# Kernel tuning notes

Hardware: AMD Instinct MI355X
Metric: run time of the kernel (lower is better)

## Reference

```python
import jax, jax.numpy as jnp
import numpy as np

N = 100000      # num nodes
E = 1600000     # num edges
F_IN = 128
F_OUT = 128
BN_EPS = 1e-5


def setup_inputs() -> dict:
    key = jax.random.key(0)
    ks = jax.random.split(key, 8)
    x = jax.random.normal(ks[0], (N, F_IN), dtype=jnp.float32)
    edge_index = jax.random.randint(ks[1], (2, E), 0, N, dtype=jnp.int64)
    # GIN learnable epsilon (init 0.0)
    eps = jnp.zeros((), dtype=jnp.float32)
    # MLP: Linear(F_IN->F_OUT) -> BatchNorm1d -> ReLU -> Linear(F_OUT->F_OUT)
    lim1 = 1.0 / np.sqrt(F_IN)
    W1 = jax.random.uniform(ks[2], (F_OUT, F_IN), minval=-lim1, maxval=lim1, dtype=jnp.float32)
    b1 = jax.random.uniform(ks[3], (F_OUT,), minval=-lim1, maxval=lim1, dtype=jnp.float32)
    gamma = jnp.ones((F_OUT,), dtype=jnp.float32)
    beta = jnp.zeros((F_OUT,), dtype=jnp.float32)
    lim2 = 1.0 / np.sqrt(F_OUT)
    W2 = jax.random.uniform(ks[4], (F_OUT, F_OUT), minval=-lim2, maxval=lim2, dtype=jnp.float32)
    b2 = jax.random.uniform(ks[5], (F_OUT,), minval=-lim2, maxval=lim2, dtype=jnp.float32)
    return {"x": x, "edge_index": edge_index, "eps": eps,
            "W1": W1, "b1": b1, "gamma": gamma, "beta": beta,
            "W2": W2, "b2": b2}


def reference(x, edge_index, eps, W1, b1, gamma, beta, W2, b2):
    row, col = edge_index[0], edge_index[1]
    # gather neighbor features and scatter-add into destination nodes
    agg = jax.ops.segment_sum(x[col], row, num_segments=x.shape[0])  # [N, F_IN]
    h = (1.0 + eps) * x + agg
    # Linear 1
    h = h @ W1.T + b1  # [N, F_OUT]
    # BatchNorm1d (training mode: batch stats over nodes, biased variance)
    mu = jnp.mean(h, axis=0)
    var = jnp.mean(jnp.square(h - mu), axis=0)
    h = (h - mu) * jax.lax.rsqrt(var + BN_EPS) * gamma + beta
    h = jax.nn.relu(h)
    # Linear 2
    return h @ W2.T + b2
```

## Files before the change

### kernel.cpp

```cpp
#include <hip/hip_runtime.h>


#define F 128
#define NPB 64
#define CLCAP 3072

typedef __attribute__((ext_vector_type(8))) short short8;
typedef __attribute__((ext_vector_type(4))) float float4v;

__device__ inline float b2f(unsigned short u) {
    union { unsigned int i; float f; } v; v.i = ((unsigned int)u) << 16; return v.f;
}
__device__ inline unsigned short f2b(float f) {
    union { float f; unsigned int i; } v; v.f = f;
    unsigned int r = v.i + 0x7FFFu + ((v.i >> 16) & 1u);
    return (unsigned short)(r >> 16);
}

__global__ __launch_bounds__(256) void conv_kernel(const float* __restrict__ x,
                                                   unsigned short* __restrict__ xh, int total,
                                                   const float* __restrict__ W1,
                                                   const float* __restrict__ W2,
                                                   unsigned short* __restrict__ w1h,
                                                   unsigned short* __restrict__ w2h,
                                                   int* __restrict__ bucketCnt, int nbuk,
                                                   float* __restrict__ stats) {
    int t = blockIdx.x * 256 + threadIdx.x;
    int i = t * 8;
    if (i < total) {
        float4 v0 = *(const float4*)(x + i);
        float4 v1 = *(const float4*)(x + i + 4);
        short8 o;
        o[0] = (short)f2b(v0.x); o[1] = (short)f2b(v0.y); o[2] = (short)f2b(v0.z); o[3] = (short)f2b(v0.w);
        o[4] = (short)f2b(v1.x); o[5] = (short)f2b(v1.y); o[6] = (short)f2b(v1.z); o[7] = (short)f2b(v1.w);
        *(short8*)(xh + i) = o;
    }
    if (t < F * F) {
        w1h[t] = f2b(W1[t]);
        w2h[t] = f2b(W2[t]);
    }
    if (blockIdx.x == 0) {
        for (int k = threadIdx.x; k < nbuk; k += 256) bucketCnt[k] = 0;
    } else if (blockIdx.x == 1) {
        if (threadIdx.x < 256) stats[threadIdx.x] = 0.f;
    }
}

__global__ __launch_bounds__(256) void bucket_hist_kernel(const int* __restrict__ rows,
                                                          int* __restrict__ bucketCnt,
                                                          int E, int nbuk) {
    extern __shared__ int bh[];
    int tid = threadIdx.x;
    for (int i = tid; i < nbuk; i += 256) bh[i] = 0;
    __syncthreads();
    int stride = gridDim.x * 256;
    for (int i = blockIdx.x * 256 + tid; i < E; i += stride)
        atomicAdd(&bh[rows[i] >> 6], 1);
    __syncthreads();
    for (int b = tid; b < nbuk; b += 256) {
        int c = bh[b];
        if (c) atomicAdd(&bucketCnt[b], c);
    }
}

__global__ void scan_buckets_kernel(const int* __restrict__ bucketCnt, int* __restrict__ bOffs,
                                    int* __restrict__ gcursor, int nbuk) {
    const int SEG = 7;
    __shared__ int tmp[256];
    int t = threadIdx.x;
    int base = t * SEG;
    int v[SEG], s = 0;
#pragma unroll
    for (int j = 0; j < SEG; j++) {
        int idx = base + j;
        v[j] = (idx < nbuk) ? bucketCnt[idx] : 0;
        s += v[j];
    }
    tmp[t] = s;
    __syncthreads();
    for (int off = 1; off < 256; off <<= 1) {
        int u = (t >= off) ? tmp[t - off] : 0;
        __syncthreads();
        tmp[t] += u;
        __syncthreads();
    }
    int run = tmp[t] - s;
#pragma unroll
    for (int j = 0; j < SEG; j++) {
        int idx = base + j;
        if (idx < nbuk) { bOffs[idx] = run; gcursor[idx] = run; }
        run += v[j];
    }
    if (t == 255) bOffs[nbuk] = tmp[255];
}

__global__ __launch_bounds__(1024) void binned_scatter_kernel(const int* __restrict__ rows,
                                                              const int* __restrict__ cols,
                                                              int* __restrict__ gcursor,
                                                              int* __restrict__ recbuf,
                                                              int E, int nbuk) {
    extern __shared__ int sm[];
    int* bh = sm;
    int* gb = sm + nbuk;
    int tid = threadIdx.x;
    int chunk = (E + gridDim.x - 1) / gridDim.x;
    int e0 = blockIdx.x * chunk;
    int e1 = min(E, e0 + chunk);
    for (int i = tid; i < nbuk; i += 1024) bh[i] = 0;
    __syncthreads();
    for (int i = e0 + tid; i < e1; i += 1024)
        atomicAdd(&bh[rows[i] >> 6], 1);
    __syncthreads();
    for (int b = tid; b < nbuk; b += 1024) {
        int c = bh[b];
        gb[b] = c ? atomicAdd(&gcursor[b], c) : 0;
        bh[b] = 0;
    }
    __syncthreads();
    for (int i = e0 + tid; i < e1; i += 1024) {
        int r = rows[i], c = cols[i];
        int k = r >> 6;
        int rk = atomicAdd(&bh[k], 1);
        recbuf[gb[k] + rk] = (c << 6) | (r & 63);
    }
}

__global__ __launch_bounds__(256) void sort_agg_kernel(const int* __restrict__ recbuf,
                                                       const int* __restrict__ bOffs,
                                                       const unsigned short* __restrict__ xh,
                                                       const float* __restrict__ epsPtr,
                                                       unsigned short* __restrict__ h0h,
                                                       int* __restrict__ clist,
                                                       int n, int nbuk) {
    __shared__ int hist[NPB];
    __shared__ int cur[NPB];
    __shared__ int offs_s[NPB + 1];
    __shared__ int cl[CLCAP];
    int b = blockIdx.x, tid = threadIdx.x;
    int base = bOffs[b];
    int cnt = bOffs[b + 1] - base;
    if (tid < NPB) hist[tid] = 0;
    __syncthreads();
    for (int i = tid; i < cnt; i += 256) atomicAdd(&hist[recbuf[base + i] & 63], 1);
    __syncthreads();
    if (tid < 64) {
        int h = hist[tid], v = h;
#pragma unroll
        for (int off = 1; off < 64; off <<= 1) {
            int u = __shfl_up(v, off, 64);
            if (tid >= off) v += u;
        }
        cur[tid] = v - h;
        offs_s[tid] = v - h;
        if (tid == 63) offs_s[64] = v;
    }
    __syncthreads();
    bool inlds = (cnt <= CLCAP);
    if (inlds) {
        for (int i = tid; i < cnt; i += 256) {
            int r = recbuf[base + i];
            int p = atomicAdd(&cur[r & 63], 1);
            cl[p] = r >> 6;
        }
    } else {
        for (int i = tid; i < cnt; i += 256) {
            int r = recbuf[base + i];
            int p = atomicAdd(&cur[r & 63], 1);
            clist[base + p] = r >> 6;
        }
    }
    __syncthreads();

    int wv = tid >> 6, lane = tid & 63;
    int qt = lane >> 4;
    int c16 = lane & 15;
    const short8* xh8 = (const short8*)xh;
    float sc = 1.0f + epsPtr[0];
    const int* glist = clist + base;
    for (int nd = wv; nd < NPB; nd += 4) {
        int node = b * NPB + nd;
        if (node >= n) break;
        int s = offs_s[nd], e = offs_s[nd + 1];
        float acc[8];
#pragma unroll
        for (int j = 0; j < 8; j++) acc[j] = 0.f;
        int i = s;
        for (; i + 16 <= e; i += 16) {
            int c[4];
#pragma unroll
            for (int u = 0; u < 4; u++) {
                int idx = i + 4 * u + qt;
                c[u] = inlds ? cl[idx] : glist[idx];
            }
            short8 v[4];
#pragma unroll
            for (int u = 0; u < 4; u++) v[u] = xh8[(size_t)c[u] * 16 + c16];
#pragma unroll
            for (int u = 0; u < 4; u++)
#pragma unroll
                for (int j = 0; j < 8; j++) acc[j] += b2f((unsigned short)v[u][j]);
        }
        if (i < e) {
            int c[4];
#pragma unroll
            for (int u = 0; u < 4; u++) {
                int idx = i + 4 * u + qt;
                c[u] = (idx < e) ? (inlds ? cl[idx] : glist[idx]) : -1;
            }
            short8 v[4];
#pragma unroll
            for (int u = 0; u < 4; u++)
                v[u] = xh8[(size_t)(c[u] < 0 ? 0 : c[u]) * 16 + c16];
#pragma unroll
            for (int u = 0; u < 4; u++) {
                if (c[u] >= 0) {
#pragma unroll
                    for (int j = 0; j < 8; j++) acc[j] += b2f((unsigned short)v[u][j]);
                }
            }
        }
#pragma unroll
        for (int j = 0; j < 8; j++) {
            acc[j] += __shfl_xor(acc[j], 16, 64);
            acc[j] += __shfl_xor(acc[j], 32, 64);
        }
        if (qt == 0) {
            short8 xv = xh8[(size_t)node * 16 + c16];
            short8 o;
#pragma unroll
            for (int j = 0; j < 8; j++) {
                float r = fmaf(sc, b2f((unsigned short)xv[j]), acc[j]);
                o[j] = (short)f2b(r);
            }
            ((short8*)h0h)[(size_t)node * 16 + c16] = o;
        }
    }
}

#define WLD 136
__global__ __launch_bounds__(256, 2) void gemm1_mfma_kernel(const unsigned short* __restrict__ h0h,
                                                            const unsigned short* __restrict__ w1h,
                                                            const float* __restrict__ b1,
                                                            unsigned short* __restrict__ h1h,
                                                            float* __restrict__ stats, int n) {
    __shared__ unsigned short wl[128 * WLD];
    __shared__ float red[4 * 256];
    int tid = threadIdx.x;
    for (int i = tid; i < 128 * 16; i += 256) {
        int r = i >> 4, ch = i & 15;
        *(short8*)(wl + r * WLD + ch * 8) = *(const short8*)(w1h + r * 128 + ch * 8);
    }
    __syncthreads();

    int wv = tid >> 6, lane = tid & 63;
    int q = lane >> 4, c15 = lane & 15;
    int rowbase = blockIdx.x * 64 + wv * 16;
    int arow = rowbase + c15; if (arow >= n) arow = n - 1;
    const unsigned short* aptr = h0h + (size_t)arow * 128 + q * 8;

    float4v acc[8];
#pragma unroll
    for (int nt = 0; nt < 8; nt++) {
        float bb = b1[nt * 16 + c15];
        acc[nt] = (float4v){bb, bb, bb, bb};
    }
#pragma unroll
    for (int ks = 0; ks < 4; ks++) {
        short8 a = *(const short8*)(aptr + ks * 32);
        const unsigned short* wp = wl + q * 8 + ks * 32;
#pragma unroll
        for (int nt = 0; nt < 8; nt++) {
            short8 b = *(const short8*)(wp + (nt * 16 + c15) * WLD);
            acc[nt] = __builtin_amdgcn_mfma_f32_16x16x32_bf16(a, b, acc[nt], 0, 0, 0);
        }
    }

    float sum[8], sq[8];
#pragma unroll
    for (int nt = 0; nt < 8; nt++) {
        sum[nt] = 0.f; sq[nt] = 0.f;
#pragma unroll
        for (int r = 0; r < 4; r++) {
            int row = rowbase + q * 4 + r;
            if (row < n) {
                float v = acc[nt][r];
                h1h[(size_t)row * 128 + nt * 16 + c15] = f2b(v);
                sum[nt] += v; sq[nt] += v * v;
            }
        }
        sum[nt] += __shfl_xor(sum[nt], 16, 64);
        sum[nt] += __shfl_xor(sum[nt], 32, 64);
        sq[nt]  += __shfl_xor(sq[nt], 16, 64);
        sq[nt]  += __shfl_xor(sq[nt], 32, 64);
    }
    if (lane < 16) {
#pragma unroll
        for (int nt = 0; nt < 8; nt++) {
            red[wv * 256 + nt * 16 + c15] = sum[nt];
            red[wv * 256 + 128 + nt * 16 + c15] = sq[nt];
        }
    }
    __syncthreads();
    if (wv == 0) {
        for (int c = lane; c < 128; c += 64) {
            float S = red[c] + red[256 + c] + red[512 + c] + red[768 + c];
            float Q = red[128 + c] + red[384 + c] + red[640 + c] + red[896 + c];
            atomicAdd(&stats[c], S);
            atomicAdd(&stats[128 + c], Q);
        }
    }
}

__global__ __launch_bounds__(256, 2) void gemm2_mfma_kernel(const unsigned short* __restrict__ h1h,
                                                            const unsigned short* __restrict__ w2h,
                                                            const float* __restrict__ b2,
                                                            const float* __restrict__ stats,
                                                            const float* __restrict__ gamma,
                                                            const float* __restrict__ beta,
                                                            float* __restrict__ out, int n) {
    __shared__ unsigned short wl[128 * WLD];
    __shared__ float ssl[256];
    int tid = threadIdx.x;
    for (int i = tid; i < 128 * 16; i += 256) {
        int r = i >> 4, ch = i & 15;
        *(short8*)(wl + r * WLD + ch * 8) = *(const short8*)(w2h + r * 128 + ch * 8);
    }
    if (tid < 128) {
        float inv_n = 1.0f / (float)n;
        float mu = stats[tid] * inv_n;
        float var = stats[F + tid] * inv_n - mu * mu;
        var = fmaxf(var, 0.0f);
        float rs = rsqrtf(var + 1e-5f);
        float s = gamma[tid] * rs;
        ssl[tid] = s;
        ssl[F + tid] = beta[tid] - mu * s;
    }
    __syncthreads();

    int wv = tid >> 6, lane = tid & 63;
    int q = lane >> 4, c15 = lane & 15;
    int rowbase = blockIdx.x * 64 + wv * 16;
    int arow = rowbase + c15; if (arow >= n) arow = n - 1;
    const unsigned short* aptr = h1h + (size_t)arow * 128 + q * 8;

    float4v acc[8];
#pragma unroll
    for (int nt = 0; nt < 8; nt++) {
        float bb = b2[nt * 16 + c15];
        acc[nt] = (float4v){bb, bb, bb, bb};
    }
#pragma unroll
    for (int ks = 0; ks < 4; ks++) {
        short8 araw = *(const short8*)(aptr + ks * 32);
        const float* ssp = ssl + ks * 32 + q * 8;
        float4 s0 = *(const float4*)(ssp);
        float4 s1 = *(const float4*)(ssp + 4);
        float4 t0 = *(const float4*)(ssp + 128);
        float4 t1 = *(const float4*)(ssp + 132);
        short8 a;
        a[0] = (short)f2b(fmaxf(fmaf(b2f((unsigned short)araw[0]), s0.x, t0.x), 0.f));
        a[1] = (short)f2b(fmaxf(fmaf(b2f((unsigned short)araw[1]), s0.y, t0.y), 0.f));
        a[2] = (short)f2b(fmaxf(fmaf(b2f((unsigned short)araw[2]), s0.z, t0.z), 0.f));
        a[3] = (short)f2b(fmaxf(fmaf(b2f((unsigned short)araw[3]), s0.w, t0.w), 0.f));
        a[4] = (short)f2b(fmaxf(fmaf(b2f((unsigned short)araw[4]), s1.x, t1.x), 0.f));
        a[5] = (short)f2b(fmaxf(fmaf(b2f((unsigned short)araw[5]), s1.y, t1.y), 0.f));
        a[6] = (short)f2b(fmaxf(fmaf(b2f((unsigned short)araw[6]), s1.z, t1.z), 0.f));
        a[7] = (short)f2b(fmaxf(fmaf(b2f((unsigned short)araw[7]), s1.w, t1.w), 0.f));
        const unsigned short* wp = wl + q * 8 + ks * 32;
#pragma unroll
        for (int nt = 0; nt < 8; nt++) {
            short8 b = *(const short8*)(wp + (nt * 16 + c15) * WLD);
            acc[nt] = __builtin_amdgcn_mfma_f32_16x16x32_bf16(a, b, acc[nt], 0, 0, 0);
        }
    }
#pragma unroll
    for (int nt = 0; nt < 8; nt++) {
#pragma unroll
        for (int r = 0; r < 4; r++) {
            int row = rowbase + q * 4 + r;
            if (row < n)
                out[(size_t)row * 128 + nt * 16 + c15] = acc[nt][r];
        }
    }
}

extern "C" void kernel_launch(void* const* d_in, const int* in_sizes, int n_in,
                              void* d_out, int out_size, void* d_ws, size_t ws_size,
                              hipStream_t stream) {
    const float* x     = (const float*)d_in[0];
    const int*   ei    = (const int*)d_in[1];
    const float* eps   = (const float*)d_in[2];
    const float* W1    = (const float*)d_in[3];
    const float* b1    = (const float*)d_in[4];
    const float* gamma = (const float*)d_in[5];
    const float* beta  = (const float*)d_in[6];
    const float* W2    = (const float*)d_in[7];
    const float* b2    = (const float*)d_in[8];
    float* out = (float*)d_out;

    const int E = in_sizes[1] / 2;
    const int n = in_sizes[0] / F;
    const int nbuk = (n + NPB - 1) / NPB;

    char* w = (char*)d_ws;
    auto alloc = [&](size_t bytes) -> void* {
        void* p = (void*)w;
        w += (bytes + 255) & ~(size_t)255;
        return p;
    };
    int*            bucketCnt = (int*)alloc((size_t)nbuk * 4);
    int*            bOffs     = (int*)alloc((size_t)(nbuk + 1) * 4);
    int*            gcursor   = (int*)alloc((size_t)nbuk * 4);
    float*          stats     = (float*)alloc(256 * 4);
    unsigned short* w1h       = (unsigned short*)alloc(F * F * 2);
    unsigned short* w2h       = (unsigned short*)alloc(F * F * 2);
    int*            recbuf    = (int*)alloc((size_t)E * 4);
    int*            clist     = (int*)alloc((size_t)E * 4);
    unsigned short* xh        = (unsigned short*)alloc((size_t)n * F * 2);
    unsigned short* h0h       = (unsigned short*)alloc((size_t)n * F * 2);
    unsigned short* h1h       = (unsigned short*)alloc((size_t)n * F * 2);

    const int* rows = ei;
    const int* cols = ei + E;

    conv_kernel<<<(n * F / 8 + 255) / 256, 256, 0, stream>>>(x, xh, n * F, W1, W2, w1h, w2h,
                                                             bucketCnt, nbuk, stats);
    bucket_hist_kernel<<<512, 256, nbuk * 4, stream>>>(rows, bucketCnt, E, nbuk);
    scan_buckets_kernel<<<1, 256, 0, stream>>>(bucketCnt, bOffs, gcursor, nbuk);
    binned_scatter_kernel<<<384, 1024, nbuk * 8, stream>>>(rows, cols, gcursor, recbuf, E, nbuk);
    sort_agg_kernel<<<nbuk, 256, 0, stream>>>(recbuf, bOffs, xh, eps, h0h, clist, n, nbuk);

    int ntiles = (n + 63) / 64;
    gemm1_mfma_kernel<<<ntiles, 256, 0, stream>>>(h0h, w1h, b1, h1h, stats, n);
    gemm2_mfma_kernel<<<ntiles, 256, 0, stream>>>(h1h, w2h, b2, stats, gamma, beta, out, n);
}
```

Before: 297.5 us.

## Replace atomic bucket cursors with per-block histogram matrix and column scan

The edge binning now has each of 256 blocks write its own per-bucket histogram into a 2D array. A new column-scan kernel turns that array into per-block exclusive offsets and bucket totals. The scatter kernel then reads its precomputed offsets instead of re-histogramming its chunk and taking global atomic cursors. This removes the redundant second histogram pass over rows and the global atomics, and makes the bucket layout deterministic, at the cost of an extra kernel launch and a 256×nbuk intermediate array read twice.

After: 305.8 us. +2.8%, slower.

```diff
diff --git a/kernel.cpp b/kernel.cpp
--- a/kernel.cpp
+++ b/kernel.cpp
@@ -4,6 +4,7 @@
 #define F 128
 #define NPB 64
 #define CLCAP 3072
+#define PB 256
 
 typedef __attribute__((ext_vector_type(8))) short short8;
 typedef __attribute__((ext_vector_type(4))) float float4v;
@@ -23,7 +24,6 @@
                                                    const float* __restrict__ W2,
                                                    unsigned short* __restrict__ w1h,
                                                    unsigned short* __restrict__ w2h,
-                                                   int* __restrict__ bucketCnt, int nbuk,
                                                    float* __restrict__ stats) {
     int t = blockIdx.x * 256 + threadIdx.x;
     int i = t * 8;
@@ -39,32 +39,53 @@
         w1h[t] = f2b(W1[t]);
         w2h[t] = f2b(W2[t]);
     }
-    if (blockIdx.x == 0) {
-        for (int k = threadIdx.x; k < nbuk; k += 256) bucketCnt[k] = 0;
-    } else if (blockIdx.x == 1) {
-        if (threadIdx.x < 256) stats[threadIdx.x] = 0.f;
-    }
-}
-
-__global__ __launch_bounds__(256) void bucket_hist_kernel(const int* __restrict__ rows,
-                                                          int* __restrict__ bucketCnt,
-                                                          int E, int nbuk) {
+    if (blockIdx.x == 0 && threadIdx.x < 256) stats[threadIdx.x] = 0.f;
+}
+
+__global__ __launch_bounds__(1024) void part_hist_kernel(const int* __restrict__ rows,
+                                                         int* __restrict__ hist2d,
+                                                         int E, int nbuk) {
     extern __shared__ int bh[];
     int tid = threadIdx.x;
-    for (int i = tid; i < nbuk; i += 256) bh[i] = 0;
-    __syncthreads();
-    int stride = gridDim.x * 256;
-    for (int i = blockIdx.x * 256 + tid; i < E; i += stride)
+    for (int i = tid; i < nbuk; i += 1024) bh[i] = 0;
+    __syncthreads();
+    int chunk = (E + gridDim.x - 1) / gridDim.x;
+    int e0 = blockIdx.x * chunk;
+    int e1 = min(E, e0 + chunk);
+    for (int i = e0 + tid; i < e1; i += 1024)
         atomicAdd(&bh[rows[i] >> 6], 1);
     __syncthreads();
-    for (int b = tid; b < nbuk; b += 256) {
-        int c = bh[b];
-        if (c) atomicAdd(&bucketCnt[b], c);
+    int* out = hist2d + (size_t)blockIdx.x * nbuk;
+    for (int b = tid; b < nbuk; b += 1024) out[b] = bh[b];
+}
+
+__global__ __launch_bounds__(256) void colscan_kernel(int* __restrict__ hist2d,
+                                                      int* __restrict__ bucketCnt, int nbuk) {
+    __shared__ int gs[4][64];
+    int lb = threadIdx.x & 63, g = threadIdx.x >> 6;
+    int b = blockIdx.x * 64 + lb;
+    int s = 0;
+    if (b < nbuk)
+        for (int j = g * 64; j < (g + 1) * 64; j++) s += hist2d[(size_t)j * nbuk + b];
+    gs[g][lb] = s;
+    __syncthreads();
+    int base = 0;
+    for (int gg = 0; gg < g; gg++) base += gs[gg][lb];
+    if (g == 0 && b < nbuk)
+        bucketCnt[b] = gs[0][lb] + gs[1][lb] + gs[2][lb] + gs[3][lb];
+    if (b < nbuk) {
+        int run = base;
+        for (int j = g * 64; j < (g + 1) * 64; j++) {
+            size_t idx = (size_t)j * nbuk + b;
+            int v = hist2d[idx];
+            hist2d[idx] = run;
+            run += v;
+        }
     }
 }
 
 __global__ void scan_buckets_kernel(const int* __restrict__ bucketCnt, int* __restrict__ bOffs,
-                                    int* __restrict__ gcursor, int nbuk) {
+                                    int nbuk) {
     const int SEG = 7;
     __shared__ int tmp[256];
     int t = threadIdx.x;
@@ -88,35 +109,31 @@
 #pragma unroll
     for (int j = 0; j < SEG; j++) {
         int idx = base + j;
-        if (idx < nbuk) { bOffs[idx] = run; gcursor[idx] = run; }
+        if (idx < nbuk) bOffs[idx] = run;
         run += v[j];
     }
     if (t == 255) bOffs[nbuk] = tmp[255];
 }
 
-__global__ __launch_bounds__(1024) void binned_scatter_kernel(const int* __restrict__ rows,
-                                                              const int* __restrict__ cols,
-                                                              int* __restrict__ gcursor,
-                                                              int* __restrict__ recbuf,
-                                                              int E, int nbuk) {
+__global__ __launch_bounds__(1024) void part_scatter_kernel(const int* __restrict__ rows,
+                                                            const int* __restrict__ cols,
+                                                            const int* __restrict__ hist2d,
+                                                            const int* __restrict__ bOffs,
+                                                            int* __restrict__ recbuf,
+                                                            int E, int nbuk) {
     extern __shared__ int sm[];
-    int* bh = sm;
-    int* gb = sm + nbuk;
+    int* gb = sm;
+    int* bh = sm + nbuk;
     int tid = threadIdx.x;
+    const int* pre = hist2d + (size_t)blockIdx.x * nbuk;
+    for (int b = tid; b < nbuk; b += 1024) {
+        gb[b] = bOffs[b] + pre[b];
+        bh[b] = 0;
+    }
+    __syncthreads();
     int chunk = (E + gridDim.x - 1) / gridDim.x;
     int e0 = blockIdx.x * chunk;
     int e1 = min(E, e0 + chunk);
-    for (int i = tid; i < nbuk; i += 1024) bh[i] = 0;
-    __syncthreads();
-    for (int i = e0 + tid; i < e1; i += 1024)
-        atomicAdd(&bh[rows[i] >> 6], 1);
-    __syncthreads();
-    for (int b = tid; b < nbuk; b += 1024) {
-        int c = bh[b];
-        gb[b] = c ? atomicAdd(&gcursor[b], c) : 0;
-        bh[b] = 0;
-    }
-    __syncthreads();
     for (int i = e0 + tid; i < e1; i += 1024) {
         int r = rows[i], c = cols[i];
         int k = r >> 6;
@@ -410,7 +427,7 @@
     };
     int*            bucketCnt = (int*)alloc((size_t)nbuk * 4);
     int*            bOffs     = (int*)alloc((size_t)(nbuk + 1) * 4);
-    int*            gcursor   = (int*)alloc((size_t)nbuk * 4);
+    int*            hist2d    = (int*)alloc((size_t)PB * nbuk * 4);
     float*          stats     = (float*)alloc(256 * 4);
     unsigned short* w1h       = (unsigned short*)alloc(F * F * 2);
     unsigned short* w2h       = (unsigned short*)alloc(F * F * 2);
@@ -423,11 +440,11 @@
     const int* rows = ei;
     const int* cols = ei + E;
 
-    conv_kernel<<<(n * F / 8 + 255) / 256, 256, 0, stream>>>(x, xh, n * F, W1, W2, w1h, w2h,
-                                                             bucketCnt, nbuk, stats);
-    bucket_hist_kernel<<<512, 256, nbuk * 4, stream>>>(rows, bucketCnt, E, nbuk);
-    scan_buckets_kernel<<<1, 256, 0, stream>>>(bucketCnt, bOffs, gcursor, nbuk);
-    binned_scatter_kernel<<<384, 1024, nbuk * 8, stream>>>(rows, cols, gcursor, recbuf, E, nbuk);
+    conv_kernel<<<(n * F / 8 + 255) / 256, 256, 0, stream>>>(x, xh, n * F, W1, W2, w1h, w2h, stats);
+    part_hist_kernel<<<PB, 1024, nbuk * 4, stream>>>(rows, hist2d, E, nbuk);
+    colscan_kernel<<<(nbuk + 63) / 64, 256, 0, stream>>>(hist2d, bucketCnt, nbuk);
+    scan_buckets_kernel<<<1, 256, 0, stream>>>(bucketCnt, bOffs, nbuk);
+    part_scatter_kernel<<<PB, 1024, nbuk * 8, stream>>>(rows, cols, hist2d, bOffs, recbuf, E, nbuk);
     sort_agg_kernel<<<nbuk, 256, 0, stream>>>(recbuf, bOffs, xh, eps, h0h, clist, n, nbuk);
 
     int ntiles = (n + 63) / 64;
```
